# Performance work log

Measured on AMD Instinct MI355X. Metric: run time of the kernel, lower is better.

Reference implementation:

```python
import jax, jax.numpy as jnp
import numpy as np

N = 262144      # total nodes
E = 1048576     # total edges
G = 8192        # num graphs (= batch[-1]+1)
H = 128         # hidden
L = 4           # layers
VA = 64         # atom feature vocab
VB = 8          # bond feature vocab
FA = 9          # atom feature columns
FB = 3          # bond feature columns
BN_EPS = 1e-5


def _bn(x, g, b, m, v):
    # BatchNorm1d in eval mode: running stats
    return (x - m) * jax.lax.rsqrt(v + BN_EPS) * g + b


def setup_inputs() -> dict:
    key = jax.random.key(0)
    ks = jax.random.split(key, 40)
    rn = lambda k, s, sc=0.05: jax.random.normal(k, s, dtype=jnp.float32) * sc
    x = jax.random.randint(ks[0], (N, FA), 0, VA)
    edge_index = jax.random.randint(ks[1], (2, E), 0, N)
    edge_attr = jax.random.randint(ks[2], (E, FB), 0, VB)
    batch = jnp.sort(jax.random.randint(ks[3], (N,), 0, G))
    batch = batch.at[0].set(0).at[-1].set(G - 1)
    params = dict(
        atom_emb=rn(ks[4], (FA, VA, H)),
        vn_emb=rn(ks[5], (H,)),
        bond_emb=rn(ks[6], (L, FB, VB, H)),
        conv_eps=rn(ks[7], (L,)),
        conv_W1=rn(ks[8], (L, H, 2 * H)), conv_b1=rn(ks[9], (L, 2 * H)),
        conv_bn_g=1.0 + rn(ks[10], (L, 2 * H)), conv_bn_b=rn(ks[11], (L, 2 * H)),
        conv_bn_m=rn(ks[12], (L, 2 * H), 0.1),
        conv_bn_v=0.5 + jax.random.uniform(ks[13], (L, 2 * H)) * 0.5,
        conv_W2=rn(ks[14], (L, 2 * H, H)), conv_b2=rn(ks[15], (L, H)),
        vn1_W=rn(ks[16], (L, 2 * H, 2 * H)), vn1_b=rn(ks[17], (L, 2 * H)),
        vn1_g=1.0 + rn(ks[18], (L, 2 * H)), vn1_be=rn(ks[19], (L, 2 * H)),
        vn1_m=rn(ks[20], (L, 2 * H), 0.1),
        vn1_v=0.5 + jax.random.uniform(ks[21], (L, 2 * H)) * 0.5,
        vn2_W=rn(ks[22], (L, 2 * H, H)), vn2_b=rn(ks[23], (L, H)),
        vn2_g=1.0 + rn(ks[24], (L, H)), vn2_be=rn(ks[25], (L, H)),
        vn2_m=rn(ks[26], (L, H), 0.1),
        vn2_v=0.5 + jax.random.uniform(ks[27], (L, H)) * 0.5,
        pW1=rn(ks[28], (H, H)), pb1=rn(ks[29], (H,)),
        pW2=rn(ks[30], (H, 1)), pb2=rn(ks[31], (1,)),
    )
    return dict(x=x, edge_index=edge_index, edge_attr=edge_attr, batch=batch, **params)


def reference(x, edge_index, edge_attr, batch, atom_emb, vn_emb, bond_emb,
              conv_eps, conv_W1, conv_b1, conv_bn_g, conv_bn_b, conv_bn_m, conv_bn_v,
              conv_W2, conv_b2, vn1_W, vn1_b, vn1_g, vn1_be, vn1_m, vn1_v,
              vn2_W, vn2_b, vn2_g, vn2_be, vn2_m, vn2_v, pW1, pb1, pW2, pb2):
    src, dst = edge_index[0], edge_index[1]
    # AtomEncoder: sum of per-feature embeddings -> [N, H]
    h = atom_emb[jnp.arange(FA)[:, None], x.T].sum(0)
    # virtual node embedding broadcast to all graphs: [G, H]
    vn = jnp.broadcast_to(vn_emb, (G, H))
    for i in range(L):
        h = h + vn[batch]
        # CombConv (GIN-with-edge-features): msg = relu(x_j + bond_emb)
        e = bond_emb[i][jnp.arange(FB)[:, None], edge_attr.T].sum(0)  # [E, H]
        msg = jax.nn.relu(h[src] + e)
        agg = jax.ops.segment_sum(msg, dst, num_segments=N)  # [N, H]
        z = (1.0 + conv_eps[i]) * h + agg
        z = jax.nn.relu(_bn(z @ conv_W1[i] + conv_b1[i],
                            conv_bn_g[i], conv_bn_b[i], conv_bn_m[i], conv_bn_v[i]))
        h = z @ conv_W2[i] + conv_b2[i]
        # virtual node update: gather-concat-MLP, pool, MLP
        t = jnp.concatenate([vn[batch], h], axis=-1)  # [N, 2H]
        t = jax.nn.relu(_bn(t @ vn1_W[i] + vn1_b[i],
                            vn1_g[i], vn1_be[i], vn1_m[i], vn1_v[i]))
        pooled = jax.ops.segment_sum(t, batch, num_segments=G)  # [G, 2H]
        vn = jax.nn.relu(_bn(pooled @ vn2_W[i] + vn2_b[i],
                             vn2_g[i], vn2_be[i], vn2_m[i], vn2_v[i]))
    # JK='L': last virtual-node representation; dropout=0
    out = jax.nn.relu(vn @ pW1 + pb1) @ pW2 + pb2  # [G, 1]
    return jnp.clip(out, 0.0, 50.0)  # eval-mode clamp
```

## Files before the change

### kernel.cpp

```cpp
#include <hip/hip_runtime.h>
#include <hip/hip_fp16.h>

#define NN 262144
#define EE 1048576
#define GG 8192
#define HH 128
#define FBc 3
#define VAc 64
#define VBc 8
#define FAc 9

typedef _Float16 f16;
typedef _Float16 f16x8 __attribute__((ext_vector_type(8)));
typedef float f32x4 __attribute__((ext_vector_type(4)));

__device__ __forceinline__ float h2f(ushort u) {
    __half h; *(ushort*)&h = u; return __half2float(h);
}
__device__ __forceinline__ ushort f2h(float f) {
    __half h = __float2half_rn(f); return *(ushort*)&h;
}
__device__ __forceinline__ int swz(int col, int row) {
    return (((col >> 3) ^ (row & 7)) << 3) | (col & 7);
}

__global__ void k_zero(float* __restrict__ p) {
    size_t i = (size_t)(blockIdx.x * 256 + threadIdx.x) * 4;
    *(float4*)(p + i) = make_float4(0.f, 0.f, 0.f, 0.f);
}

__global__ void k_atom(const int* __restrict__ x, const float* __restrict__ emb,
                       ushort* __restrict__ h16) {
    int t = blockIdx.x * 256 + threadIdx.x;
    int n = t >> 5, c = (t & 31) << 2;
    if (n >= NN) return;
    float4 a = make_float4(0.f, 0.f, 0.f, 0.f);
#pragma unroll
    for (int f = 0; f < FAc; ++f) {
        int v = x[n * FAc + f];
        float4 e = *(const float4*)(emb + ((size_t)(f * VAc + v)) * HH + c);
        a.x += e.x; a.y += e.y; a.z += e.z; a.w += e.w;
    }
    ushort4 o;
    o.x = f2h(a.x * 0.0625f); o.y = f2h(a.y * 0.0625f);
    o.z = f2h(a.z * 0.0625f); o.w = f2h(a.w * 0.0625f);
    *(ushort4*)(h16 + (size_t)n * HH + c) = o;
}

__global__ void k_hist(const int* __restrict__ ei, int* __restrict__ deg) {
    int e = blockIdx.x * 256 + threadIdx.x;
    atomicAdd(&deg[ei[EE + e]], 1);
}
__global__ void k_scan1(const int* __restrict__ deg, int* __restrict__ rowptr,
                        int* __restrict__ sums) {
    __shared__ int s[256];
    int base = blockIdx.x * 1024 + threadIdx.x * 4;
    int4 d = *(const int4*)(deg + base);
    int t = d.x + d.y + d.z + d.w;
    s[threadIdx.x] = t;
    __syncthreads();
    for (int off = 1; off < 256; off <<= 1) {
        int v = (threadIdx.x >= off) ? s[threadIdx.x - off] : 0;
        __syncthreads();
        s[threadIdx.x] += v;
        __syncthreads();
    }
    int excl = s[threadIdx.x] - t;
    int4 o; o.x = excl; o.y = excl + d.x; o.z = o.y + d.y; o.w = o.z + d.z;
    *(int4*)(rowptr + base) = o;
    if (threadIdx.x == 255) sums[blockIdx.x] = s[255];
}
__global__ void k_scan2(int* __restrict__ sums) {
    __shared__ int s[256];
    int t = sums[threadIdx.x];
    s[threadIdx.x] = t;
    __syncthreads();
    for (int off = 1; off < 256; off <<= 1) {
        int v = (threadIdx.x >= off) ? s[threadIdx.x - off] : 0;
        __syncthreads();
        s[threadIdx.x] += v;
        __syncthreads();
    }
    sums[threadIdx.x] = s[threadIdx.x] - t;
}
__global__ void k_scan3(int* __restrict__ rowptr, const int* __restrict__ sums,
                        int* __restrict__ fill) {
    int base = blockIdx.x * 1024 + threadIdx.x * 4;
    int add = sums[blockIdx.x];
    int4 r = *(const int4*)(rowptr + base);
    r.x += add; r.y += add; r.z += add; r.w += add;
    *(int4*)(rowptr + base) = r;
    *(int4*)(fill + base) = r;
    if (blockIdx.x == 0 && threadIdx.x == 0) rowptr[NN] = EE;
}
__global__ void k_scatter(const int* __restrict__ ei, const int* __restrict__ ea,
                          int* __restrict__ fill, unsigned* __restrict__ packed) {
    int e = blockIdx.x * 256 + threadIdx.x;
    int dst = ei[EE + e];
    int pos = atomicAdd(&fill[dst], 1);
    unsigned cb = (unsigned)(ea[e * 3 + 0] + ea[e * 3 + 1] * 8 + ea[e * 3 + 2] * 64);
    packed[pos] = (unsigned)ei[e] | (cb << 18);
}
__global__ void k_gstart(const int* __restrict__ batch, int* __restrict__ gstart) {
    int n = blockIdx.x * 256 + threadIdx.x;
    if (n >= NN) return;
    int b0 = batch[n];
    int b1 = (n + 1 < NN) ? batch[n + 1] : GG;
    if (n == 0) gstart[0] = 0;
    for (int g = b0 + 1; g <= b1; ++g) gstart[g] = n + 1;
}

__global__ void k_setup_all(
    const float* __restrict__ bond_emb, ushort* __restrict__ ct16_all,
    const float* __restrict__ conv_b1, const float* __restrict__ cbn_g,
    const float* __restrict__ cbn_b, const float* __restrict__ cbn_m,
    const float* __restrict__ cbn_v,
    const float* __restrict__ vn1_g, const float* __restrict__ vn1_be,
    const float* __restrict__ vn1_m, const float* __restrict__ vn1_v,
    const float* __restrict__ vn2_g, const float* __restrict__ vn2_be,
    const float* __restrict__ vn2_m, const float* __restrict__ vn2_v,
    const float* __restrict__ vn2_b,
    float* __restrict__ tabs,
    const float* __restrict__ conv_W1, ushort* __restrict__ W1t_all,
    const float* __restrict__ conv_W2, ushort* __restrict__ W2t_all,
    const float* __restrict__ vn1_W,  ushort* __restrict__ W3t_all) {
    int layer = blockIdx.x / 449;
    int t = (blockIdx.x % 449) * 256 + threadIdx.x;
    if (t < 16384) {
        const float* bemb = bond_emb + (size_t)layer * FBc * VBc * HH;
        int cb = t >> 5, c = (t & 31) << 2;
        int a0 = cb & 7, a1 = (cb >> 3) & 7, a2 = cb >> 6;
        float4 b0 = *(const float4*)(bemb + (size_t)(0 * VBc + a0) * HH + c);
        float4 b1v = *(const float4*)(bemb + (size_t)(1 * VBc + a1) * HH + c);
        float4 b2v = *(const float4*)(bemb + (size_t)(2 * VBc + a2) * HH + c);
        ushort4 o;
        o.x = f2h((b0.x + b1v.x + b2v.x) * 0.0625f);
        o.y = f2h((b0.y + b1v.y + b2v.y) * 0.0625f);
        o.z = f2h((b0.z + b1v.z + b2v.z) * 0.0625f);
        o.w = f2h((b0.w + b1v.w + b2v.w) * 0.0625f);
        *(ushort4*)(ct16_all + (size_t)layer * 512 * HH + (size_t)cb * HH + c) = o;
    } else if (t < 16640) {
        int c = t - 16384;
        float* T = tabs + (size_t)layer * 1536;
        float s1 = cbn_g[layer * 256 + c] * rsqrtf(cbn_v[layer * 256 + c] + 1e-5f);
        T[0 * 256 + c] = s1;
        T[1 * 256 + c] = ((conv_b1[layer * 256 + c] - cbn_m[layer * 256 + c]) * s1
                          + cbn_b[layer * 256 + c]) * 0.0625f;
        float s3 = vn1_g[layer * 256 + c] * rsqrtf(vn1_v[layer * 256 + c] + 1e-5f);
        T[2 * 256 + c] = 16.f * s3;
        T[3 * 256 + c] = vn1_be[layer * 256 + c] - vn1_m[layer * 256 + c] * s3;
        T[4 * 256 + c] = s3;
        if (c < 128) {
            float s2 = vn2_g[layer * 128 + c] * rsqrtf(vn2_v[layer * 128 + c] + 1e-5f);
            T[5 * 256 + c] = s2;
            T[5 * 256 + 128 + c] = (vn2_b[layer * 128 + c] - vn2_m[layer * 128 + c]) * s2
                                   + vn2_be[layer * 128 + c];
        }
    } else if (t < 49408) {
        int o = t - 16640;
        int c = o >> 7, k = o & 127;
        W1t_all[(size_t)layer * 32768 + o] =
            f2h(conv_W1[(size_t)layer * 128 * 256 + (size_t)k * 256 + c]);
    } else if (t < 82176) {
        int o = t - 49408;
        int c = o >> 8, k = o & 255;
        W2t_all[(size_t)layer * 32768 + o] =
            f2h(conv_W2[(size_t)layer * 256 * 128 + (size_t)k * 128 + c]);
    } else if (t < 114944) {
        int o = t - 82176;
        int c = o >> 7, k = o & 127;
        W3t_all[(size_t)layer * 32768 + o] =
            f2h(vn1_W[(size_t)layer * 256 * 256 + 128 * 256 + (size_t)k * 256 + c]);
    }
}

template <int MODE>
__global__ void __launch_bounds__(256)
k_vn(float* __restrict__ pooled, const float* __restrict__ vn_emb,
     const float* __restrict__ vn2W_prev,
     const float* __restrict__ tab_prev,
     const float* __restrict__ vn1W_cur,
     const float* __restrict__ vn1b_cur,
     const float* __restrict__ tab_cur,
     float* __restrict__ vn_out, float* __restrict__ vnW,
     const ushort* __restrict__ h16, ushort* __restrict__ hb16,
     const int* __restrict__ gstart, const int* __restrict__ batch) {
    __shared__ float pl[16][256];
    __shared__ float vnL[16][128];
    const int tid = threadIdx.x;
    const int g0 = blockIdx.x * 16;

    if (MODE != 0) {
        for (int i = tid; i < 1024; i += 256) {
            int r = i >> 6, c4 = (i & 63) << 2;
            *(float4*)&pl[r][c4] = *(const float4*)(pooled + (size_t)(g0 + r) * 256 + c4);
        }
        __syncthreads();
        {
            int r = tid >> 4, c0 = (tid & 15) * 8;
            float acc[8] = {};
            for (int k = 0; k < 256; ++k) {
                float a = pl[r][k];
                const float* wr = vn2W_prev + (size_t)k * 128 + c0;
                float4 w0 = *(const float4*)wr, w1 = *(const float4*)(wr + 4);
                acc[0] += a * w0.x; acc[1] += a * w0.y; acc[2] += a * w0.z; acc[3] += a * w0.w;
                acc[4] += a * w1.x; acc[5] += a * w1.y; acc[6] += a * w1.z; acc[7] += a * w1.w;
            }
            const float* VA = tab_prev + 5 * 256;
            const float* VB = VA + 128;
#pragma unroll
            for (int j = 0; j < 8; ++j)
                vnL[r][c0 + j] = fmaxf(acc[j] * VA[c0 + j] + VB[c0 + j], 0.f);
        }
    } else {
        for (int i = tid; i < 2048; i += 256) {
            int r = i >> 7, c = i & 127;
            vnL[r][c] = vn_emb[c];
        }
    }
    __syncthreads();
    for (int i = tid; i < 512; i += 256) {
        int r = i >> 5, c4 = (i & 31) << 2;
        *(float4*)(vn_out + (size_t)(g0 + r) * 128 + c4) = *(const float4*)&vnL[r][c4];
    }
    if (MODE == 2) return;

    {
        int r = tid >> 4, c0 = (tid & 15) * 16;
        float acc[16] = {};
        for (int k = 0; k < 128; ++k) {
            float a = vnL[r][k];
            const float* wr = vn1W_cur + (size_t)k * 256 + c0;
#pragma unroll
            for (int j4 = 0; j4 < 4; ++j4) {
                float4 w = *(const float4*)(wr + j4 * 4);
                acc[j4 * 4 + 0] += a * w.x; acc[j4 * 4 + 1] += a * w.y;
                acc[j4 * 4 + 2] += a * w.z; acc[j4 * 4 + 3] += a * w.w;
            }
        }
        const float* S3 = tab_cur + 4 * 256;
#pragma unroll
        for (int j = 0; j < 16; ++j)
            vnW[(size_t)(g0 + r) * 256 + c0 + j] =
                (acc[j] + vn1b_cur[c0 + j]) * S3[c0 + j];
    }
    for (int i = tid; i < 1024; i += 256) {
        int r = i >> 6, c4 = (i & 63) << 2;
        *(float4*)(pooled + (size_t)(g0 + r) * 256 + c4) = make_float4(0.f, 0.f, 0.f, 0.f);
    }
    {
        int nn0 = gstart[g0], nn1 = gstart[g0 + 16];
        for (int q = nn0 * 4 + tid; q < nn1 * 4; q += 256) {
            int n = q >> 2, ch0 = (q & 3) * 32;
            int g = batch[n] - g0;
#pragma unroll
            for (int j4 = 0; j4 < 4; ++j4) {
                f16x8 hv = *(const f16x8*)(h16 + (size_t)n * HH + ch0 + j4 * 8);
                f16x8 o;
#pragma unroll
                for (int j = 0; j < 8; ++j)
                    o[j] = (f16)((float)hv[j] + vnL[g][ch0 + j4 * 8 + j] * 0.0625f);
                *(f16x8*)(hb16 + (size_t)n * HH + ch0 + j4 * 8) = o;
            }
        }
    }
}

__global__ void __launch_bounds__(256, 3)
k_conv(ushort* __restrict__ h16, const ushort* __restrict__ hb16,
       const int* __restrict__ rowptr, const unsigned* __restrict__ packed,
       const ushort* __restrict__ ct16,
       const ushort* __restrict__ W1t, const ushort* __restrict__ W2t,
       const ushort* __restrict__ W3t,
       const int* __restrict__ batch, const float* __restrict__ vnW,
       const float* __restrict__ eps_ptr, const float* __restrict__ tabs,
       const float* __restrict__ b2,
       float* __restrict__ pooled) {
    __shared__ ushort zs[64][256];
    __shared__ ushort Wb[64][128];
    ushort(*Wb2)[256] = (ushort(*)[256]) & Wb[0][0];
    const int tid = threadIdx.x;
    const int r0 = blockIdx.x * 64;
    const int w = tid >> 6, l = tid & 63, lr = l & 15, lg = l >> 4, lr7 = lr & 7;
    const float eps1 = 1.f + eps_ptr[0];
    const int myrow = w * 16 + lr;
    const int growA = r0 + myrow;
    const float* ZA = tabs;
    const float* ZB = tabs + 256;
    const float* TA = tabs + 512;
    const float* TB = tabs + 768;
    int rl[4], ggs[4];
#pragma unroll
    for (int reg = 0; reg < 4; ++reg) {
        rl[reg] = w * 16 + lg * 4 + reg;
        ggs[reg] = batch[r0 + rl[reg]];
    }

    {
        int grp = tid >> 4, ln = tid & 15;
        int ch0 = ln * 8;
        for (int rr = 0; rr < 4; ++rr) {
            int row = grp * 4 + rr;
            int beg = rowptr[r0 + row], end = rowptr[r0 + row + 1];
            float ac[8] = {0.f, 0.f, 0.f, 0.f, 0.f, 0.f, 0.f, 0.f};
            int e = beg;
            for (; e + 3 < end; e += 4) {
                unsigned p0 = packed[e], p1 = packed[e + 1];
                unsigned p2 = packed[e + 2], p3 = packed[e + 3];
                f16x8 h0 = *(const f16x8*)(hb16 + (size_t)(p0 & 0x3FFFF) * HH + ch0);
                f16x8 h1 = *(const f16x8*)(hb16 + (size_t)(p1 & 0x3FFFF) * HH + ch0);
                f16x8 h2 = *(const f16x8*)(hb16 + (size_t)(p2 & 0x3FFFF) * HH + ch0);
                f16x8 h3 = *(const f16x8*)(hb16 + (size_t)(p3 & 0x3FFFF) * HH + ch0);
                f16x8 t0 = *(const f16x8*)(ct16 + (size_t)(p0 >> 18) * HH + ch0);
                f16x8 t1 = *(const f16x8*)(ct16 + (size_t)(p1 >> 18) * HH + ch0);
                f16x8 t2 = *(const f16x8*)(ct16 + (size_t)(p2 >> 18) * HH + ch0);
                f16x8 t3 = *(const f16x8*)(ct16 + (size_t)(p3 >> 18) * HH + ch0);
#pragma unroll
                for (int j = 0; j < 8; ++j) {
                    ac[j] += fmaxf((float)h0[j] + (float)t0[j], 0.f)
                           + fmaxf((float)h1[j] + (float)t1[j], 0.f)
                           + fmaxf((float)h2[j] + (float)t2[j], 0.f)
                           + fmaxf((float)h3[j] + (float)t3[j], 0.f);
                }
            }
            for (; e < end; ++e) {
                unsigned p = packed[e];
                f16x8 hv = *(const f16x8*)(hb16 + (size_t)(p & 0x3FFFF) * HH + ch0);
                f16x8 ct = *(const f16x8*)(ct16 + (size_t)(p >> 18) * HH + ch0);
#pragma unroll
                for (int j = 0; j < 8; ++j)
                    ac[j] += fmaxf((float)hv[j] + (float)ct[j], 0.f);
            }
            f16x8 o;
#pragma unroll
            for (int j = 0; j < 8; ++j) o[j] = (f16)ac[j];
            *(f16x8*)&zs[row][((ch0 >> 3) ^ (row & 7)) << 3] = o;
        }
    }
    __syncthreads();

    f16x8 af[4];
#pragma unroll
    for (int k0 = 0; k0 < 4; ++k0) {
        int ko = k0 * 32 + lg * 8;
        f16x8 hb = *(const f16x8*)(hb16 + (size_t)growA * HH + ko);
        f16x8 ag = *(const f16x8*)&zs[myrow][((ko >> 3) ^ (myrow & 7)) << 3];
#pragma unroll
        for (int j = 0; j < 8; ++j)
            af[k0][j] = (f16)(eps1 * (float)hb[j] + (float)ag[j]);
    }

    for (int qt = 0; qt < 4; ++qt) {
        __syncthreads();
        {
            int c = tid >> 2, q = tid & 3, c7 = c & 7;
            const ushort* s = W1t + (size_t)(qt * 64 + c) * 128 + q * 32;
#pragma unroll
            for (int j4 = 0; j4 < 4; ++j4)
                *(f16x8*)&Wb[c][((q * 4 + j4) ^ c7) << 3] = *(const f16x8*)(s + j4 * 8);
        }
        __syncthreads();
        f32x4 acc[4] = {};
        __builtin_amdgcn_s_setprio(1);
#pragma unroll
        for (int k0 = 0; k0 < 4; ++k0) {
            int sb = ((k0 * 4 + lg) ^ lr7) << 3;
#pragma unroll
            for (int fc = 0; fc < 4; ++fc) {
                f16x8 bf = *(const f16x8*)&Wb[fc * 16 + lr][sb];
                acc[fc] = __builtin_amdgcn_mfma_f32_16x16x32_f16(af[k0], bf, acc[fc], 0, 0, 0);
            }
        }
        __builtin_amdgcn_s_setprio(0);
#pragma unroll
        for (int fc = 0; fc < 4; ++fc) {
            int col = qt * 64 + fc * 16 + lr;
            float za = ZA[col], zb = ZB[col];
#pragma unroll
            for (int reg = 0; reg < 4; ++reg) {
                float zv = fmaxf(acc[fc][reg] * za + zb, 0.f);
                zs[rl[reg]][swz(col, rl[reg])] = f2h(zv);
            }
        }
    }

    f32x4 acc2[8] = {};
    for (int st = 0; st < 4; ++st) {
        __syncthreads();
        {
            int c = tid >> 3, q = tid & 7, c7 = c & 7;
            const ushort* s = W2t + (size_t)(st * 32 + c) * 256 + q * 32;
#pragma unroll
            for (int j4 = 0; j4 < 4; ++j4)
                *(f16x8*)&Wb2[c][((q * 4 + j4) ^ c7) << 3] = *(const f16x8*)(s + j4 * 8);
        }
        __syncthreads();
        __builtin_amdgcn_s_setprio(1);
#pragma unroll
        for (int k0 = 0; k0 < 8; ++k0) {
            int sb = ((k0 * 4 + lg) ^ lr7) << 3;
            f16x8 az = *(const f16x8*)&zs[myrow][sb];
#pragma unroll
            for (int fc = 0; fc < 2; ++fc) {
                f16x8 bf = *(const f16x8*)&Wb2[fc * 16 + lr][sb];
                acc2[st * 2 + fc] =
                    __builtin_amdgcn_mfma_f32_16x16x32_f16(az, bf, acc2[st * 2 + fc], 0, 0, 0);
            }
        }
        __builtin_amdgcn_s_setprio(0);
    }
    __syncthreads();
#pragma unroll
    for (int st = 0; st < 4; ++st) {
#pragma unroll
        for (int fc = 0; fc < 2; ++fc) {
            int col = st * 32 + fc * 16 + lr;
            float bb = b2[col];
#pragma unroll
            for (int reg = 0; reg < 4; ++reg) {
                float hv = acc2[st * 2 + fc][reg] * 16.f + bb;
                zs[rl[reg]][swz(col, rl[reg])] = f2h(hv * 0.0625f);
            }
        }
    }
    {
        int row = tid >> 2, q = tid & 3, r7 = row & 7;
#pragma unroll
        for (int j4 = 0; j4 < 4; ++j4) {
            f16x8 v = *(const f16x8*)&zs[row][((q * 4 + j4) ^ r7) << 3];
            *(f16x8*)(h16 + (size_t)(r0 + row) * HH + q * 32 + j4 * 8) = v;
        }
    }

    for (int pr = 0; pr < 2; ++pr) {
#pragma unroll
        for (int sub = 0; sub < 2; ++sub) {
            int qt = pr * 2 + sub;
            __syncthreads();
            {
                int c = tid >> 2, q = tid & 3, c7 = c & 7;
                const ushort* s = W3t + (size_t)(qt * 64 + c) * 128 + q * 32;
#pragma unroll
                for (int j4 = 0; j4 < 4; ++j4)
                    *(f16x8*)&Wb[c][((q * 4 + j4) ^ c7) << 3] = *(const f16x8*)(s + j4 * 8);
            }
            __syncthreads();
            f32x4 acc3[4] = {};
            __builtin_amdgcn_s_setprio(1);
#pragma unroll
            for (int k0 = 0; k0 < 4; ++k0) {
                int sb = ((k0 * 4 + lg) ^ lr7) << 3;
                f16x8 ah = *(const f16x8*)&zs[myrow][sb];
#pragma unroll
                for (int fc = 0; fc < 4; ++fc) {
                    f16x8 bf = *(const f16x8*)&Wb[fc * 16 + lr][sb];
                    acc3[fc] = __builtin_amdgcn_mfma_f32_16x16x32_f16(ah, bf, acc3[fc], 0, 0, 0);
                }
            }
            __builtin_amdgcn_s_setprio(0);
#pragma unroll
            for (int fc = 0; fc < 4; ++fc) {
                int colg = qt * 64 + fc * 16 + lr;
                int colL = 128 + sub * 64 + fc * 16 + lr;
                float ta = TA[colg], tb = TB[colg];
#pragma unroll
                for (int reg = 0; reg < 4; ++reg) {
                    float tv = fmaxf(acc3[fc][reg] * ta + vnW[(size_t)ggs[reg] * 256 + colg] + tb, 0.f);
                    zs[rl[reg]][swz(colL, rl[reg])] = f2h(tv);
                }
            }
        }
        __syncthreads();
        {
            int c = tid & 127, half = tid >> 7;
            int gcol = pr * 128 + c;
            int colL = 128 + c;
            float s = 0.f;
            int cur = batch[r0 + half * 32];
            for (int r = half * 32; r < half * 32 + 32; ++r) {
                int gg = batch[r0 + r];
                if (gg != cur) {
                    atomicAdd(&pooled[(size_t)cur * 256 + gcol], s);
                    s = 0.f; cur = gg;
                }
                s += h2f(zs[r][swz(colL, r)]);
            }
            atomicAdd(&pooled[(size_t)cur * 256 + gcol], s);
        }
        __syncthreads();
    }
}

__global__ void k_final(const float* __restrict__ vn, const float* __restrict__ pW1,
                        const float* __restrict__ pb1, const float* __restrict__ pW2,
                        const float* __restrict__ pb2, float* __restrict__ out) {
    int g = blockIdx.x;
    int j = threadIdx.x;
    __shared__ float vrow[HH];
    __shared__ float red[HH];
    vrow[j] = vn[(size_t)g * HH + j];
    __syncthreads();
    float acc = pb1[j];
    for (int k = 0; k < HH; ++k) acc = fmaf(vrow[k], pW1[k * HH + j], acc);
    red[j] = fmaxf(acc, 0.f) * pW2[j];
    __syncthreads();
    for (int s = 64; s > 0; s >>= 1) {
        if (j < s) red[j] += red[j + s];
        __syncthreads();
    }
    if (j == 0) out[g] = fminf(fmaxf(red[0] + pb2[0], 0.f), 50.f);
}

extern "C" void kernel_launch(void* const* d_in, const int* in_sizes, int n_in,
                              void* d_out, int out_size, void* d_ws, size_t ws_size,
                              hipStream_t stream) {
    const int*   x        = (const int*)  d_in[0];
    const int*   ei       = (const int*)  d_in[1];
    const int*   ea       = (const int*)  d_in[2];
    const int*   batch    = (const int*)  d_in[3];
    const float* atom_emb = (const float*)d_in[4];
    const float* vn_emb   = (const float*)d_in[5];
    const float* bond_emb = (const float*)d_in[6];
    const float* conv_eps = (const float*)d_in[7];
    const float* conv_W1  = (const float*)d_in[8];
    const float* conv_b1  = (const float*)d_in[9];
    const float* cbn_g    = (const float*)d_in[10];
    const float* cbn_b    = (const float*)d_in[11];
    const float* cbn_m    = (const float*)d_in[12];
    const float* cbn_v    = (const float*)d_in[13];
    const float* conv_W2  = (const float*)d_in[14];
    const float* conv_b2  = (const float*)d_in[15];
    const float* vn1_W    = (const float*)d_in[16];
    const float* vn1_b    = (const float*)d_in[17];
    const float* vn1_g    = (const float*)d_in[18];
    const float* vn1_be   = (const float*)d_in[19];
    const float* vn1_m    = (const float*)d_in[20];
    const float* vn1_v    = (const float*)d_in[21];
    const float* vn2_W    = (const float*)d_in[22];
    const float* vn2_b    = (const float*)d_in[23];
    const float* vn2_g    = (const float*)d_in[24];
    const float* vn2_be   = (const float*)d_in[25];
    const float* vn2_m    = (const float*)d_in[26];
    const float* vn2_v    = (const float*)d_in[27];
    const float* pW1      = (const float*)d_in[28];
    const float* pb1      = (const float*)d_in[29];
    const float* pW2      = (const float*)d_in[30];
    const float* pb2      = (const float*)d_in[31];

    char* base = (char*)d_ws;
    ushort*   h16     = (ushort*)base;
    ushort*   hb16    = h16 + (size_t)NN * HH;
    unsigned* packed  = (unsigned*)(hb16 + (size_t)NN * HH);
    int*      rowptr  = (int*)(packed + EE);
    int*      fill    = rowptr + NN + 4;
    int*      gstart  = fill + NN;
    int*      sums    = gstart + GG + 8;
    ushort*   ct16a   = (ushort*)(sums + 256);
    ushort*   W1ta    = ct16a + 4 * 512 * HH;
    ushort*   W2ta    = W1ta + 4 * 32768;
    ushort*   W3ta    = W2ta + 4 * 32768;
    float*    tabs    = (float*)(W3ta + 4 * 32768);
    float*    vn      = tabs + 4 * 1536;
    float*    vnW     = vn + (size_t)GG * HH;
    float*    pooled  = vnW + (size_t)GG * 256;
    float*    out     = (float*)d_out;

    k_zero<<<256, 256, 0, stream>>>((float*)fill);
    k_hist<<<EE / 256, 256, 0, stream>>>(ei, fill);
    k_scan1<<<256, 256, 0, stream>>>(fill, rowptr, sums);
    k_scan2<<<1, 256, 0, stream>>>(sums);
    k_scan3<<<256, 256, 0, stream>>>(rowptr, sums, fill);
    k_scatter<<<EE / 256, 256, 0, stream>>>(ei, ea, fill, packed);
    k_gstart<<<NN / 256, 256, 0, stream>>>(batch, gstart);
    k_atom<<<NN * 32 / 256, 256, 0, stream>>>(x, atom_emb, h16);
    k_setup_all<<<4 * 449, 256, 0, stream>>>(
        bond_emb, ct16a,
        conv_b1, cbn_g, cbn_b, cbn_m, cbn_v,
        vn1_g, vn1_be, vn1_m, vn1_v,
        vn2_g, vn2_be, vn2_m, vn2_v, vn2_b,
        tabs, conv_W1, W1ta, conv_W2, W2ta, vn1_W, W3ta);

    for (int i = 0; i < 4; ++i) {
        if (i == 0) {
            k_vn<0><<<GG / 16, 256, 0, stream>>>(
                pooled, vn_emb, nullptr, nullptr,
                vn1_W + (size_t)i * 256 * 256, vn1_b + i * 256, tabs + (size_t)i * 1536,
                vn, vnW, h16, hb16, gstart, batch);
        } else {
            k_vn<1><<<GG / 16, 256, 0, stream>>>(
                pooled, nullptr,
                vn2_W + (size_t)(i - 1) * 256 * 128, tabs + (size_t)(i - 1) * 1536,
                vn1_W + (size_t)i * 256 * 256, vn1_b + i * 256, tabs + (size_t)i * 1536,
                vn, vnW, h16, hb16, gstart, batch);
        }
        k_conv<<<NN / 64, 256, 0, stream>>>(
            h16, hb16, rowptr, packed,
            ct16a + (size_t)i * 512 * HH,
            W1ta + (size_t)i * 32768, W2ta + (size_t)i * 32768, W3ta + (size_t)i * 32768,
            batch, vnW, conv_eps + i, tabs + (size_t)i * 1536,
            conv_b2 + i * HH, pooled);
    }
    k_vn<2><<<GG / 16, 256, 0, stream>>>(
        pooled, nullptr,
        vn2_W + (size_t)3 * 256 * 128, tabs + (size_t)3 * 1536,
        nullptr, nullptr, nullptr,
        vn, nullptr, nullptr, nullptr, nullptr, nullptr);
    k_final<<<GG, 128, 0, stream>>>(vn, pW1, pb1, pW2, pb2, out);
}
```

Before: 1.690 ms.

## Replace fused virtual-node kernel with tiled SMEM GEMMs and separate hb16 kernel

Drops the per-16-graph k_vn kernel. The virtual-node MLPs now run as a generic 64x64 shared-memory-tiled fp32 GEMM with bias/BN-ReLU epilogues, and the vn[batch]+h broadcast moves into a separate node-parallel k_hb16 kernel; gstart is no longer needed. The old kernel streamed weights from global memory per thread and walked each graph's nodes inside a small block, so it had poor weight reuse and uneven work per block. The cost is more kernel launches per layer and extra round trips through global memory for vn, vnW and pooled zeroing.

Result: faster. 1.466 ms (-13.2%).

```diff
diff --git a/kernel.cpp b/kernel.cpp
--- a/kernel.cpp
+++ b/kernel.cpp
@@ -45,6 +45,27 @@
     o.x = f2h(a.x * 0.0625f); o.y = f2h(a.y * 0.0625f);
     o.z = f2h(a.z * 0.0625f); o.w = f2h(a.w * 0.0625f);
     *(ushort4*)(h16 + (size_t)n * HH + c) = o;
+}
+
+__global__ void k_init_vn(const float* __restrict__ vn_emb, float* __restrict__ vn) {
+    int t = blockIdx.x * 256 + threadIdx.x;
+    int g = t >> 5, c = (t & 31) << 2;
+    *(float4*)(vn + (size_t)g * HH + c) = *(const float4*)(vn_emb + c);
+}
+
+__global__ void k_hb16(const ushort* __restrict__ h16, const float* __restrict__ vn,
+                       const int* __restrict__ batch, ushort* __restrict__ hb16) {
+    int t = blockIdx.x * 256 + threadIdx.x;
+    int n = t >> 4, ch0 = (t & 15) * 8;
+    int g = batch[n];
+    f16x8 hv = *(const f16x8*)(h16 + (size_t)n * HH + ch0);
+    const float* vp = vn + (size_t)g * HH + ch0;
+    float4 v0 = *(const float4*)vp, v1 = *(const float4*)(vp + 4);
+    float vv[8] = {v0.x, v0.y, v0.z, v0.w, v1.x, v1.y, v1.z, v1.w};
+    f16x8 o;
+#pragma unroll
+    for (int j = 0; j < 8; ++j) o[j] = (f16)((float)hv[j] + vv[j] * 0.0625f);
+    *(f16x8*)(hb16 + (size_t)n * HH + ch0) = o;
 }
 
 __global__ void k_hist(const int* __restrict__ ei, int* __restrict__ deg) {
@@ -101,14 +122,6 @@
     unsigned cb = (unsigned)(ea[e * 3 + 0] + ea[e * 3 + 1] * 8 + ea[e * 3 + 2] * 64);
     packed[pos] = (unsigned)ei[e] | (cb << 18);
 }
-__global__ void k_gstart(const int* __restrict__ batch, int* __restrict__ gstart) {
-    int n = blockIdx.x * 256 + threadIdx.x;
-    if (n >= NN) return;
-    int b0 = batch[n];
-    int b1 = (n + 1 < NN) ? batch[n + 1] : GG;
-    if (n == 0) gstart[0] = 0;
-    for (int g = b0 + 1; g <= b1; ++g) gstart[g] = n + 1;
-}
 
 __global__ void k_setup_all(
     const float* __restrict__ bond_emb, ushort* __restrict__ ct16_all,
@@ -117,9 +130,6 @@
     const float* __restrict__ cbn_v,
     const float* __restrict__ vn1_g, const float* __restrict__ vn1_be,
     const float* __restrict__ vn1_m, const float* __restrict__ vn1_v,
-    const float* __restrict__ vn2_g, const float* __restrict__ vn2_be,
-    const float* __restrict__ vn2_m, const float* __restrict__ vn2_v,
-    const float* __restrict__ vn2_b,
     float* __restrict__ tabs,
     const float* __restrict__ conv_W1, ushort* __restrict__ W1t_all,
     const float* __restrict__ conv_W2, ushort* __restrict__ W2t_all,
@@ -141,7 +151,7 @@
         *(ushort4*)(ct16_all + (size_t)layer * 512 * HH + (size_t)cb * HH + c) = o;
     } else if (t < 16640) {
         int c = t - 16384;
-        float* T = tabs + (size_t)layer * 1536;
+        float* T = tabs + (size_t)layer * 1280;
         float s1 = cbn_g[layer * 256 + c] * rsqrtf(cbn_v[layer * 256 + c] + 1e-5f);
         T[0 * 256 + c] = s1;
         T[1 * 256 + c] = ((conv_b1[layer * 256 + c] - cbn_m[layer * 256 + c]) * s1
@@ -150,12 +160,6 @@
         T[2 * 256 + c] = 16.f * s3;
         T[3 * 256 + c] = vn1_be[layer * 256 + c] - vn1_m[layer * 256 + c] * s3;
         T[4 * 256 + c] = s3;
-        if (c < 128) {
-            float s2 = vn2_g[layer * 128 + c] * rsqrtf(vn2_v[layer * 128 + c] + 1e-5f);
-            T[5 * 256 + c] = s2;
-            T[5 * 256 + 128 + c] = (vn2_b[layer * 128 + c] - vn2_m[layer * 128 + c]) * s2
-                                   + vn2_be[layer * 128 + c];
-        }
     } else if (t < 49408) {
         int o = t - 16640;
         int c = o >> 7, k = o & 127;
@@ -171,98 +175,6 @@
         int c = o >> 7, k = o & 127;
         W3t_all[(size_t)layer * 32768 + o] =
             f2h(vn1_W[(size_t)layer * 256 * 256 + 128 * 256 + (size_t)k * 256 + c]);
-    }
-}
-
-template <int MODE>
-__global__ void __launch_bounds__(256)
-k_vn(float* __restrict__ pooled, const float* __restrict__ vn_emb,
-     const float* __restrict__ vn2W_prev,
-     const float* __restrict__ tab_prev,
-     const float* __restrict__ vn1W_cur,
-     const float* __restrict__ vn1b_cur,
-     const float* __restrict__ tab_cur,
-     float* __restrict__ vn_out, float* __restrict__ vnW,
-     const ushort* __restrict__ h16, ushort* __restrict__ hb16,
-     const int* __restrict__ gstart, const int* __restrict__ batch) {
-    __shared__ float pl[16][256];
-    __shared__ float vnL[16][128];
-    const int tid = threadIdx.x;
-    const int g0 = blockIdx.x * 16;
-
-    if (MODE != 0) {
-        for (int i = tid; i < 1024; i += 256) {
-            int r = i >> 6, c4 = (i & 63) << 2;
-            *(float4*)&pl[r][c4] = *(const float4*)(pooled + (size_t)(g0 + r) * 256 + c4);
-        }
-        __syncthreads();
-        {
-            int r = tid >> 4, c0 = (tid & 15) * 8;
-            float acc[8] = {};
-            for (int k = 0; k < 256; ++k) {
-                float a = pl[r][k];
-                const float* wr = vn2W_prev + (size_t)k * 128 + c0;
-                float4 w0 = *(const float4*)wr, w1 = *(const float4*)(wr + 4);
-                acc[0] += a * w0.x; acc[1] += a * w0.y; acc[2] += a * w0.z; acc[3] += a * w0.w;
-                acc[4] += a * w1.x; acc[5] += a * w1.y; acc[6] += a * w1.z; acc[7] += a * w1.w;
-            }
-            const float* VA = tab_prev + 5 * 256;
-            const float* VB = VA + 128;
-#pragma unroll
-            for (int j = 0; j < 8; ++j)
-                vnL[r][c0 + j] = fmaxf(acc[j] * VA[c0 + j] + VB[c0 + j], 0.f);
-        }
-    } else {
-        for (int i = tid; i < 2048; i += 256) {
-            int r = i >> 7, c = i & 127;
-            vnL[r][c] = vn_emb[c];
-        }
-    }
-    __syncthreads();
-    for (int i = tid; i < 512; i += 256) {
-        int r = i >> 5, c4 = (i & 31) << 2;
-        *(float4*)(vn_out + (size_t)(g0 + r) * 128 + c4) = *(const float4*)&vnL[r][c4];
-    }
-    if (MODE == 2) return;
-
-    {
-        int r = tid >> 4, c0 = (tid & 15) * 16;
-        float acc[16] = {};
-        for (int k = 0; k < 128; ++k) {
-            float a = vnL[r][k];
-            const float* wr = vn1W_cur + (size_t)k * 256 + c0;
-#pragma unroll
-            for (int j4 = 0; j4 < 4; ++j4) {
-                float4 w = *(const float4*)(wr + j4 * 4);
-                acc[j4 * 4 + 0] += a * w.x; acc[j4 * 4 + 1] += a * w.y;
-                acc[j4 * 4 + 2] += a * w.z; acc[j4 * 4 + 3] += a * w.w;
-            }
-        }
-        const float* S3 = tab_cur + 4 * 256;
-#pragma unroll
-        for (int j = 0; j < 16; ++j)
-            vnW[(size_t)(g0 + r) * 256 + c0 + j] =
-                (acc[j] + vn1b_cur[c0 + j]) * S3[c0 + j];
-    }
-    for (int i = tid; i < 1024; i += 256) {
-        int r = i >> 6, c4 = (i & 63) << 2;
-        *(float4*)(pooled + (size_t)(g0 + r) * 256 + c4) = make_float4(0.f, 0.f, 0.f, 0.f);
-    }
-    {
-        int nn0 = gstart[g0], nn1 = gstart[g0 + 16];
-        for (int q = nn0 * 4 + tid; q < nn1 * 4; q += 256) {
-            int n = q >> 2, ch0 = (q & 3) * 32;
-            int g = batch[n] - g0;
-#pragma unroll
-            for (int j4 = 0; j4 < 4; ++j4) {
-                f16x8 hv = *(const f16x8*)(h16 + (size_t)n * HH + ch0 + j4 * 8);
-                f16x8 o;
-#pragma unroll
-                for (int j = 0; j < 8; ++j)
-                    o[j] = (f16)((float)hv[j] + vnL[g][ch0 + j4 * 8 + j] * 0.0625f);
-                *(f16x8*)(hb16 + (size_t)n * HH + ch0 + j4 * 8) = o;
-            }
-        }
     }
 }
 
@@ -488,6 +400,78 @@
             atomicAdd(&pooled[(size_t)cur * 256 + gcol], s);
         }
         __syncthreads();
+    }
+}
+
+enum { E_BIAS = 0, E_BNRELU = 1 };
+template <int EMODE>
+__global__ void __launch_bounds__(256)
+gemm_k(const void* __restrict__ Av, const float* __restrict__ B,
+       const float* __restrict__ bias,
+       const float* __restrict__ g_, const float* __restrict__ b_,
+       const float* __restrict__ m_, const float* __restrict__ v_,
+       const float* __restrict__ scp,
+       void* __restrict__ outv, int K, int Nc) {
+    __shared__ float As[64][33];
+    __shared__ float Bs[32][64];
+    const int tid = threadIdx.x;
+    const int row0 = blockIdx.x * 64;
+    const int col0 = blockIdx.y * 64;
+    float acc[4][4] = {};
+    const int tx = tid & 15, ty = tid >> 4;
+    for (int k0 = 0; k0 < K; k0 += 32) {
+#pragma unroll
+        for (int p = 0; p < 2; ++p) {
+            int idx = p * 256 + tid;
+            {
+                int r = idx >> 3, c = (idx & 7) << 2;
+                size_t aoff = (size_t)(row0 + r) * K + k0 + c;
+                float4 va = *(const float4*)((const float*)Av + aoff);
+                As[r][c + 0] = va.x; As[r][c + 1] = va.y;
+                As[r][c + 2] = va.z; As[r][c + 3] = va.w;
+            }
+            {
+                int kr = idx >> 4, cc = (idx & 15) << 2;
+                *(float4*)&Bs[kr][cc] =
+                    *(const float4*)(B + (size_t)(k0 + kr) * Nc + col0 + cc);
+            }
+        }
+        __syncthreads();
+#pragma unroll
+        for (int k = 0; k < 32; ++k) {
+            float4 bv = *(const float4*)&Bs[k][tx << 2];
+            float a0 = As[ty * 4 + 0][k];
+            float a1 = As[ty * 4 + 1][k];
+            float a2 = As[ty * 4 + 2][k];
+            float a3 = As[ty * 4 + 3][k];
+            acc[0][0] += a0 * bv.x; acc[0][1] += a0 * bv.y; acc[0][2] += a0 * bv.z; acc[0][3] += a0 * bv.w;
+            acc[1][0] += a1 * bv.x; acc[1][1] += a1 * bv.y; acc[1][2] += a1 * bv.z; acc[1][3] += a1 * bv.w;
+            acc[2][0] += a2 * bv.x; acc[2][1] += a2 * bv.y; acc[2][2] += a2 * bv.z; acc[2][3] += a2 * bv.w;
+            acc[3][0] += a3 * bv.x; acc[3][1] += a3 * bv.y; acc[3][2] += a3 * bv.z; acc[3][3] += a3 * bv.w;
+        }
+        __syncthreads();
+    }
+#pragma unroll
+    for (int j = 0; j < 4; ++j) {
+        int gr = row0 + ty * 4 + j;
+        float vals[4];
+#pragma unroll
+        for (int lx = 0; lx < 4; ++lx) {
+            int gc = col0 + (tx << 2) + lx;
+            float val = acc[j][lx];
+            if (EMODE == E_BIAS) {
+                float v = val + bias[gc];
+                if (scp) v *= scp[gc];
+                vals[lx] = v;
+            } else {
+                float y = val + bias[gc];
+                float s = g_[gc] * rsqrtf(v_[gc] + 1e-5f);
+                y = (y - m_[gc]) * s + b_[gc];
+                vals[lx] = fmaxf(y, 0.f);
+            }
+        }
+        *(float4*)((float*)outv + (size_t)gr * Nc + col0 + (tx << 2)) =
+            make_float4(vals[0], vals[1], vals[2], vals[3]);
     }
 }
 
@@ -553,14 +537,13 @@
     unsigned* packed  = (unsigned*)(hb16 + (size_t)NN * HH);
     int*      rowptr  = (int*)(packed + EE);
     int*      fill    = rowptr + NN + 4;
-    int*      gstart  = fill + NN;
-    int*      sums    = gstart + GG + 8;
+    int*      sums    = fill + NN;
     ushort*   ct16a   = (ushort*)(sums + 256);
     ushort*   W1ta    = ct16a + 4 * 512 * HH;
     ushort*   W2ta    = W1ta + 4 * 32768;
     ushort*   W3ta    = W2ta + 4 * 32768;
     float*    tabs    = (float*)(W3ta + 4 * 32768);
-    float*    vn      = tabs + 4 * 1536;
+    float*    vn      = tabs + 4 * 1280;
     float*    vnW     = vn + (size_t)GG * HH;
     float*    pooled  = vnW + (size_t)GG * 256;
     float*    out     = (float*)d_out;
@@ -571,39 +554,45 @@
     k_scan2<<<1, 256, 0, stream>>>(sums);
     k_scan3<<<256, 256, 0, stream>>>(rowptr, sums, fill);
     k_scatter<<<EE / 256, 256, 0, stream>>>(ei, ea, fill, packed);
-    k_gstart<<<NN / 256, 256, 0, stream>>>(batch, gstart);
     k_atom<<<NN * 32 / 256, 256, 0, stream>>>(x, atom_emb, h16);
+    k_init_vn<<<GG * HH / 4 / 256, 256, 0, stream>>>(vn_emb, vn);
     k_setup_all<<<4 * 449, 256, 0, stream>>>(
         bond_emb, ct16a,
         conv_b1, cbn_g, cbn_b, cbn_m, cbn_v,
         vn1_g, vn1_be, vn1_m, vn1_v,
-        vn2_g, vn2_be, vn2_m, vn2_v, vn2_b,
         tabs, conv_W1, W1ta, conv_W2, W2ta, vn1_W, W3ta);
 
     for (int i = 0; i < 4; ++i) {
-        if (i == 0) {
-            k_vn<0><<<GG / 16, 256, 0, stream>>>(
-                pooled, vn_emb, nullptr, nullptr,
-                vn1_W + (size_t)i * 256 * 256, vn1_b + i * 256, tabs + (size_t)i * 1536,
-                vn, vnW, h16, hb16, gstart, batch);
-        } else {
-            k_vn<1><<<GG / 16, 256, 0, stream>>>(
-                pooled, nullptr,
-                vn2_W + (size_t)(i - 1) * 256 * 128, tabs + (size_t)(i - 1) * 1536,
-                vn1_W + (size_t)i * 256 * 256, vn1_b + i * 256, tabs + (size_t)i * 1536,
-                vn, vnW, h16, hb16, gstart, batch);
-        }
+        if (i > 0) {
+            dim3 g4(GG / 64, 2);
+            gemm_k<E_BNRELU><<<g4, 256, 0, stream>>>(
+                pooled, vn2_W + (size_t)(i - 1) * 256 * HH, vn2_b + (i - 1) * HH,
+                vn2_g + (i - 1) * HH, vn2_be + (i - 1) * HH,
+                vn2_m + (i - 1) * HH, vn2_v + (i - 1) * HH,
+                nullptr, vn, 256, HH);
+        }
+        {
+            dim3 g3(GG / 64, 4);
+            gemm_k<E_BIAS><<<g3, 256, 0, stream>>>(
+                vn, vn1_W + (size_t)i * 256 * 256, vn1_b + i * 256,
+                nullptr, nullptr, nullptr, nullptr,
+                tabs + (size_t)i * 1280 + 4 * 256, vnW, HH, 256);
+        }
+        k_hb16<<<NN * 16 / 256, 256, 0, stream>>>(h16, vn, batch, hb16);
+        k_zero<<<GG * 256 / 4 / 256, 256, 0, stream>>>(pooled);
         k_conv<<<NN / 64, 256, 0, stream>>>(
             h16, hb16, rowptr, packed,
             ct16a + (size_t)i * 512 * HH,
             W1ta + (size_t)i * 32768, W2ta + (size_t)i * 32768, W3ta + (size_t)i * 32768,
-            batch, vnW, conv_eps + i, tabs + (size_t)i * 1536,
+            batch, vnW, conv_eps + i, tabs + (size_t)i * 1280,
             conv_b2 + i * HH, pooled);
     }
-    k_vn<2><<<GG / 16, 256, 0, stream>>>(
-        pooled, nullptr,
-        vn2_W + (size_t)3 * 256 * 128, tabs + (size_t)3 * 1536,
-        nullptr, nullptr, nullptr,
-        vn, nullptr, nullptr, nullptr, nullptr, nullptr);
+    {
+        dim3 g4(GG / 64, 2);
+        gemm_k<E_BNRELU><<<g4, 256, 0, stream>>>(
+            pooled, vn2_W + (size_t)3 * 256 * HH, vn2_b + 3 * HH,
+            vn2_g + 3 * HH, vn2_be + 3 * HH, vn2_m + 3 * HH, vn2_v + 3 * HH,
+            nullptr, vn, 256, HH);
+    }
     k_final<<<GG, 128, 0, stream>>>(vn, pW1, pb1, pW2, pb2, out);
 }
```
